# Optimization experiments

Hardware: AMD Instinct MI355X
Metric: run time of the kernel (lower is better)

Reference implementation:

```python
import jax, jax.numpy as jnp
import numpy as np

# Dimensions
B2, T, C = 400, 120, 128          # x: ((B*V), T, C)
V = 25                            # num_point (skeleton joints)
NH_A = 3                          # adjacency heads (A.shape[0])
HEADS, DH = 8, 64                 # attention heads, dim_head
INNER = HEADS * DH                # 512
QKV_C = INNER * 3                 # 1536 = GCN out_channels
EPS = 1e-5                        # torch BatchNorm2d default eps


def setup_inputs() -> dict:
    key = jax.random.key(0)
    ks = jax.random.split(key, 12)
    z = lambda *s: jnp.zeros(s, jnp.float32)
    o = lambda *s: jnp.ones(s, jnp.float32)
    return {
        "x": jax.random.normal(ks[0], (B2, T, C), jnp.float32),
        # GCN shared topology (num_head, V, V)
        "A": jax.random.normal(ks[1], (NH_A, V, V), jnp.float32) * 0.2,
        # per-head 1x1 conv weights/biases (stacked)
        "conv_w": jax.random.normal(ks[2], (NH_A, QKV_C, C), jnp.float32) * 0.02,
        "conv_b": jax.random.normal(ks[3], (NH_A, QKV_C), jnp.float32) * 0.01,
        # main BatchNorm2d (eval mode, running stats)
        "bn_gamma": jax.random.uniform(ks[4], (QKV_C,), jnp.float32, 0.5, 1.5),
        "bn_beta": z(QKV_C),
        "bn_mean": z(QKV_C),
        "bn_var": o(QKV_C),
        # down path: 1x1 conv + BatchNorm2d (in_c != out_c)
        "down_w": jax.random.normal(ks[5], (QKV_C, C), jnp.float32) * 0.02,
        "down_b": z(QKV_C),
        "dbn_gamma": jax.random.uniform(ks[6], (QKV_C,), jnp.float32, 0.5, 1.5),
        "dbn_beta": z(QKV_C),
        "dbn_mean": z(QKV_C),
        "dbn_var": o(QKV_C),
        # to_out Linear(inner_dim -> dim)
        "out_w": jax.random.normal(ks[7], (C, INNER), jnp.float32) * 0.02,
        "out_b": z(C),
    }


def _bn_eval(y, gamma, beta, mean, var):
    # y: (b, o, t, v); BN over channel axis 1, eval mode
    inv = gamma / jnp.sqrt(var + EPS)
    return y * inv[None, :, None, None] + (beta - mean * inv)[None, :, None, None]


def reference(x, A, conv_w, conv_b, bn_gamma, bn_beta, bn_mean, bn_var,
              down_w, down_b, dbn_gamma, dbn_beta, dbn_mean, dbn_var,
              out_w, out_b):
    B = B2 // V
    # '(b v) t c -> b c t v'
    x4 = x.reshape(B, V, T, C).transpose(0, 3, 2, 1)  # (b, c, t, v)

    # ---- GCN projection: sum_h Conv1x1_h(A_h @ x) ----
    z = jnp.einsum('hvu,bctu->bhctv', A, x4)                    # (b,h,c,t,v)
    y = jnp.einsum('hoc,bhctv->botv', conv_w, z)                # (b,O,t,v)
    y = y + conv_b.sum(0)[None, :, None, None]
    y = _bn_eval(y, bn_gamma, bn_beta, bn_mean, bn_var)

    d = jnp.einsum('oc,bctv->botv', down_w, x4) + down_b[None, :, None, None]
    d = _bn_eval(d, dbn_gamma, dbn_beta, dbn_mean, dbn_var)

    y = jax.nn.relu(y + d)                                      # (b,O,t,v)

    # ---- attention over time per (batch*joint) row ----
    qkv = y.transpose(0, 3, 2, 1).reshape(B2, T, QKV_C)         # '(b v) t c'
    q, k, v = jnp.split(qkv, 3, axis=-1)
    split_heads = lambda t: t.reshape(B2, T, HEADS, DH).transpose(0, 2, 1, 3)
    q, k, v = split_heads(q), split_heads(k), split_heads(v)

    dots = jnp.einsum('bhid,bhjd->bhij', q, k) * (DH ** -0.5)
    mask = jnp.tril(jnp.ones((T, T), bool))                     # causal mask
    dots = jnp.where(mask[None, None], dots, -jnp.inf)
    attn = jax.nn.softmax(dots, axis=-1)                        # (B2,H,T,T)

    o = jnp.einsum('bhij,bhjd->bhid', attn, v)
    o = o.transpose(0, 2, 1, 3).reshape(B2, T, INNER)
    out = o @ out_w.T + out_b                                   # (B2,T,C)
    return out, attn
```

## Files before the change

kernel.cpp:

```cpp
#include <hip/hip_runtime.h>


typedef __bf16 bf16;
typedef __bf16 bf16x8 __attribute__((ext_vector_type(8)));
typedef __bf16 bf16x4 __attribute__((ext_vector_type(4)));
typedef float  f32x4  __attribute__((ext_vector_type(4)));
typedef __attribute__((address_space(1))) const void* gptr1;
typedef __attribute__((address_space(3))) void*       lptr3;

#define GLL16(g, l) __builtin_amdgcn_global_load_lds((gptr1)(g), (lptr3)(l), 16, 0, 0)
#define MFMA16(a, b, c) __builtin_amdgcn_mfma_f32_16x16x32_bf16(a, b, c, 0, 0, 0)

__global__ __launch_bounds__(256) void build_weights(
    const float* __restrict__ conv_w, const float* __restrict__ conv_b,
    const float* __restrict__ g1, const float* __restrict__ be1,
    const float* __restrict__ mu1, const float* __restrict__ va1,
    const float* __restrict__ down_w, const float* __restrict__ down_b,
    const float* __restrict__ g2, const float* __restrict__ be2,
    const float* __restrict__ mu2, const float* __restrict__ va2,
    const float* __restrict__ out_w,
    bf16* __restrict__ wcat, bf16* __restrict__ wout, float* __restrict__ bias)
{
    int idx = blockIdx.x * 256 + threadIdx.x;
    if (idx < 1536 * 512) {
        int o = idx >> 9, k = idx & 511;
        float s, w;
        if (k < 384) {
            int h = k >> 7, c = k & 127;
            s = g1[o] * rsqrtf(va1[o] + 1e-5f);
            w = conv_w[(h * 1536 + o) * 128 + c];
        } else {
            s = g2[o] * rsqrtf(va2[o] + 1e-5f);
            w = down_w[o * 128 + (k - 384)];
        }
        wcat[idx] = (bf16)(w * s);
    }
    int i2 = idx - 1536 * 512;
    if (i2 >= 0 && i2 < 128 * 512) wout[i2] = (bf16)out_w[i2];
    int i3 = idx - (1536 * 512 + 128 * 512);
    if (i3 >= 0 && i3 < 1536) {
        int o = i3;
        float s1 = g1[o] * rsqrtf(va1[o] + 1e-5f);
        float s2 = g2[o] * rsqrtf(va2[o] + 1e-5f);
        float cb = conv_b[o] + conv_b[1536 + o] + conv_b[2 * 1536 + o];
        bias[o] = cb * s1 + be1[o] - mu1[o] * s1
                + down_b[o] * s2 + be2[o] - mu2[o] * s2;
    }
}

__global__ __launch_bounds__(256) void transform(
    const float* __restrict__ x, const float* __restrict__ A,
    bf16* __restrict__ zt)
{
    __shared__ float xs[25][128];
    const int tid = threadIdx.x;
    const int bt = blockIdx.x;
    const int b = bt / 120, t = bt - b * 120;
    for (int i = tid; i < 25 * 128; i += 256) {
        int u = i >> 7, c = i & 127;
        xs[u][c] = x[((size_t)(b * 25 + u) * 120 + t) * 128 + c];
    }
    __syncthreads();
    const int c = tid & 127, g = tid >> 7;
    float xr[25];
    #pragma unroll
    for (int u = 0; u < 25; u++) xr[u] = xs[u][c];
    for (int idx = g; idx < 75; idx += 2) {
        int h = idx / 25, v = idx - h * 25;
        const float* Ap = A + (h * 25 + v) * 25;
        float acc = 0.f;
        #pragma unroll
        for (int u = 0; u < 25; u++) acc += Ap[u] * xr[u];
        zt[((size_t)(b * 25 + v) * 120 + t) * 512 + h * 128 + c] = (bf16)acc;
    }
    for (int v = g; v < 25; v += 2)
        zt[((size_t)(b * 25 + v) * 120 + t) * 512 + 384 + c] = (bf16)xs[v][c];
}

__global__ __launch_bounds__(256) void gemm_qkv(
    const bf16* __restrict__ wcat, const bf16* __restrict__ zt,
    const float* __restrict__ bias,
    bf16* __restrict__ qg, bf16* __restrict__ kg, bf16* __restrict__ vtg)
{
    __shared__ __align__(16) char smem[32768];
    bf16* AsB = (bf16*)smem;
    bf16* BsB = (bf16*)(smem + 8192);
    const int tid = threadIdx.x, lane = tid & 63, wv = tid >> 6;
    const int wrow = wv >> 1, wcol = wv & 1;
    const int NB = 4500, q8 = NB >> 3, r8 = NB & 7;
    const int xcd = blockIdx.x & 7, sidx = blockIdx.x >> 3;
    const int vid = (xcd < r8 ? xcd * (q8 + 1) : r8 * (q8 + 1) + (xcd - r8) * q8) + sidx;
    const int mt = vid % 12, nt = vid / 12;
    const int colb = lane & 15, rg = lane >> 4;

    f32x4 zz = {0.f, 0.f, 0.f, 0.f};
    f32x4 acc[4][4];
    #pragma unroll
    for (int i = 0; i < 4; i++)
        #pragma unroll
        for (int j = 0; j < 4; j++) acc[i][j] = zz;

    const char* gA = (const char*)wcat + (size_t)mt * 128 * 1024;
    const char* gB = (const char*)zt + (size_t)nt * 128 * 1024;
    const int srow = lane >> 2, skb = (lane & 3) * 16;
    const int aoff0 = (wrow * 64 + colb) * 64 + rg * 16;
    const int boff0 = (wcol * 64 + colb) * 64 + rg * 16;

    for (int kt = 0; kt < 16; kt++) {
        __syncthreads();
        #pragma unroll
        for (int j = 0; j < 2; j++) {
            int ck = wv * 2 + j;
            int row = ck * 16 + srow;
            GLL16(gA + (size_t)row * 1024 + kt * 64 + skb, (char*)AsB + ck * 1024);
            GLL16(gB + (size_t)row * 1024 + kt * 64 + skb, (char*)BsB + ck * 1024);
        }
        asm volatile("s_waitcnt vmcnt(0)" ::: "memory");
        __syncthreads();
        bf16x8 af[4], bfr[4];
        #pragma unroll
        for (int m = 0; m < 4; m++)
            af[m] = *(const bf16x8*)((const char*)AsB + aoff0 + m * 1024);
        #pragma unroll
        for (int n = 0; n < 4; n++)
            bfr[n] = *(const bf16x8*)((const char*)BsB + boff0 + n * 1024);
        #pragma unroll
        for (int m = 0; m < 4; m++)
            #pragma unroll
            for (int n = 0; n < 4; n++)
                acc[m][n] = MFMA16(af[m], bfr[n], acc[m][n]);
    }

    const int mtb = mt * 128, ntb = nt * 128;
    const int which = mtb >> 9;

    if (which < 2) {
        __syncthreads();
        bf16* Lt = (bf16*)smem;
        const float qs = (which == 0) ? 0.125f : 1.0f;
        #pragma unroll
        for (int m = 0; m < 4; m++) {
            int o0 = wrow * 64 + m * 16 + rg * 4;
            float b0 = bias[mtb + o0 + 0], b1 = bias[mtb + o0 + 1];
            float b2 = bias[mtb + o0 + 2], b3 = bias[mtb + o0 + 3];
            #pragma unroll
            for (int nn = 0; nn < 4; nn++) {
                int n_ = wcol * 64 + nn * 16 + colb;
                bf16x4 pk;
                pk[0] = (bf16)(fmaxf(acc[m][nn][0] + b0, 0.f) * qs);
                pk[1] = (bf16)(fmaxf(acc[m][nn][1] + b1, 0.f) * qs);
                pk[2] = (bf16)(fmaxf(acc[m][nn][2] + b2, 0.f) * qs);
                pk[3] = (bf16)(fmaxf(acc[m][nn][3] + b3, 0.f) * qs);
                *(bf16x4*)((char*)Lt + n_ * 256 + ((o0 * 2) ^ ((n_ & 7) << 4))) = pk;
            }
        }
        __syncthreads();
        bf16* dst = (which == 0) ? qg : kg;
        #pragma unroll
        for (int i = 0; i < 8; i++) {
            int ch = i * 256 + tid;
            int n_ = ch >> 4, c16 = ch & 15;
            int ng = ntb + n_;
            int grp = ng / 120, t = ng - grp * 120;
            int o = mtb + c16 * 8;
            int hd = (o >> 6) & 7, dd0 = o & 63;
            bf16x8 vv = *(const bf16x8*)((const char*)Lt + n_ * 256 +
                                         ((c16 * 16) ^ ((n_ & 7) << 4)));
            *(bf16x8*)(dst + ((size_t)(grp * 8 + hd) * 120 + t) * 64 + dd0) = vv;
        }
    } else {
        #pragma unroll
        for (int m = 0; m < 4; m++) {
            #pragma unroll
            for (int reg = 0; reg < 4; reg++) {
                int o = mtb + wrow * 64 + m * 16 + rg * 4 + reg;
                float bo = bias[o];
                int hd = (o >> 6) & 7, dd = o & 63;
                #pragma unroll
                for (int nn = 0; nn < 4; nn++) {
                    int n = ntb + wcol * 64 + nn * 16 + colb;
                    int grp = n / 120, t = n - grp * 120;
                    float val = fmaxf(acc[m][nn][reg] + bo, 0.f);
                    vtg[((size_t)(grp * 8 + hd) * 64 + dd) * 128 + t] = (bf16)val;
                }
            }
        }
    }
}

__global__ __launch_bounds__(256) void attn_k(
    const bf16* __restrict__ qg, const bf16* __restrict__ kg,
    const bf16* __restrict__ vtg, float* __restrict__ attn_out,
    bf16* __restrict__ og)
{
    __shared__ __align__(16) bf16 Ks[128 * 64];
    __shared__ __align__(16) bf16 Vt[64 * 128];
    __shared__ __align__(16) bf16 Ps[128 * 128];
    const int tid = threadIdx.x, lane = tid & 63, wv = tid >> 6;
    const int bh = blockIdx.x;
    const int colb = lane & 15, rg = lane >> 4;

    const char* ksrc = (const char*)kg + (size_t)bh * 15360;
    const char* vsrc = (const char*)vtg + (size_t)bh * 16384;
    #pragma unroll
    for (int is = 0; is < 4; is++) {
        int cb = is * 256 + wv * 64;
        if (cb < 960) {
            int bb = (cb + lane) * 16;
            int row = bb >> 7;
            int gsrc = (bb & ~127) | ((bb & 127) ^ ((row & 7) << 4));
            GLL16(ksrc + gsrc, (char*)Ks + cb * 16);
        }
        {
            int bb = (cb + lane) * 16;
            int row = bb >> 8;
            int gsrc = (bb & ~255) | ((bb & 255) ^ ((row & 7) << 4));
            GLL16(vsrc + gsrc, (char*)Vt + cb * 16);
        }
    }
    const char* qsrc = (const char*)qg + (size_t)bh * 15360;
    bf16x8 qf[2][2];
    #pragma unroll
    for (int kk = 0; kk < 2; kk++)
        #pragma unroll
        for (int m = 0; m < 2; m++) {
            int row = wv * 32 + m * 16 + colb;
            qf[kk][m] = *(const bf16x8*)(qsrc + (size_t)row * 128 + rg * 16 + kk * 64);
        }
    asm volatile("s_waitcnt vmcnt(0)" ::: "memory");
    __syncthreads();
    {
        f32x4 z = {0.f, 0.f, 0.f, 0.f};
        if (tid < 64) {
            int r = 120 + (tid >> 3), off = (tid & 7) * 16;
            *(f32x4*)((char*)Ks + r * 128 + off) = z;
        } else if (tid < 128) {
            int d = tid - 64;
            *(f32x4*)((char*)Vt + d * 256 + (240 ^ ((d & 7) << 4))) = z;
        }
    }
    __syncthreads();

    f32x4 accs[2][8];
    #pragma unroll
    for (int m = 0; m < 2; m++)
        #pragma unroll
        for (int ct = 0; ct < 8; ct++) accs[m][ct] = (f32x4){0.f, 0.f, 0.f, 0.f};
    #pragma unroll
    for (int kk = 0; kk < 2; kk++) {
        #pragma unroll
        for (int ct = 0; ct < 8; ct++) {
            int rk = ct * 16 + colb;
            int byo = rk * 128 + ((rg * 16 + kk * 64) ^ ((rk & 7) << 4));
            bf16x8 bk = *(const bf16x8*)((const char*)Ks + byo);
            accs[0][ct] = MFMA16(qf[kk][0], bk, accs[0][ct]);
            accs[1][ct] = MFMA16(qf[kk][1], bk, accs[1][ct]);
        }
    }

    const int rqb = wv * 32;
    float* attn_base = attn_out + (size_t)bh * 120 * 120;
    #pragma unroll
    for (int m = 0; m < 2; m++) {
        #pragma unroll
        for (int reg = 0; reg < 4; reg++) {
            int t_q = rqb + m * 16 + rg * 4 + reg;
            float s[8], mx = -1e30f;
            #pragma unroll
            for (int ct = 0; ct < 8; ct++) {
                int col = ct * 16 + colb;
                bool valid = (col <= t_q) && (col < 120);
                s[ct] = valid ? accs[m][ct][reg] : -1e30f;
                mx = fmaxf(mx, s[ct]);
            }
            #pragma unroll
            for (int d = 1; d < 16; d <<= 1) mx = fmaxf(mx, __shfl_xor(mx, d, 64));
            float p[8], sum = 0.f;
            #pragma unroll
            for (int ct = 0; ct < 8; ct++) {
                p[ct] = (s[ct] > -1e29f) ? __expf(s[ct] - mx) : 0.f;
                sum += p[ct];
            }
            #pragma unroll
            for (int d = 1; d < 16; d <<= 1) sum += __shfl_xor(sum, d, 64);
            float inv = 1.f / sum;
            if (t_q < 120) {
                float* orow = attn_base + (size_t)t_q * 120;
                #pragma unroll
                for (int ct = 0; ct < 8; ct++) {
                    int col = ct * 16 + colb;
                    if (col < 120) orow[col] = p[ct] * inv;
                }
            }
            #pragma unroll
            for (int ct = 0; ct < 8; ct++) {
                int col = ct * 16 + colb;
                int byo = t_q * 256 + ((col * 2) ^ ((t_q & 7) << 4));
                *(bf16*)((char*)Ps + byo) = (bf16)(p[ct] * inv);
            }
        }
    }
    __syncthreads();

    f32x4 acco[2][4];
    #pragma unroll
    for (int m = 0; m < 2; m++)
        #pragma unroll
        for (int dt = 0; dt < 4; dt++) acco[m][dt] = (f32x4){0.f, 0.f, 0.f, 0.f};
    for (int kk = 0; kk <= wv; kk++) {
        bf16x8 ap[2];
        #pragma unroll
        for (int m = 0; m < 2; m++) {
            int row = rqb + m * 16 + colb;
            int byo = row * 256 + ((rg * 16 + kk * 64) ^ ((row & 7) << 4));
            ap[m] = *(const bf16x8*)((const char*)Ps + byo);
        }
        #pragma unroll
        for (int dt = 0; dt < 4; dt++) {
            int rd = dt * 16 + colb;
            int byo = rd * 256 + ((rg * 16 + kk * 64) ^ ((rd & 7) << 4));
            bf16x8 bv = *(const bf16x8*)((const char*)Vt + byo);
            acco[0][dt] = MFMA16(ap[0], bv, acco[0][dt]);
            acco[1][dt] = MFMA16(ap[1], bv, acco[1][dt]);
        }
    }
    const int b2 = bh >> 3, h = bh & 7;
    #pragma unroll
    for (int m = 0; m < 2; m++)
        #pragma unroll
        for (int dt = 0; dt < 4; dt++)
            #pragma unroll
            for (int reg = 0; reg < 4; reg++) {
                int t = rqb + m * 16 + rg * 4 + reg;
                if (t < 120) {
                    int dfull = h * 64 + dt * 16 + colb;
                    og[((size_t)b2 * 120 + t) * 512 + dfull] = (bf16)acco[m][dt][reg];
                }
            }
}

__global__ __launch_bounds__(256) void gemm_out_k(
    const bf16* __restrict__ og, const bf16* __restrict__ wout,
    const float* __restrict__ outb, float* __restrict__ out)
{
    __shared__ __align__(16) bf16 As[128 * 32];
    __shared__ __align__(16) bf16 Bs[128 * 32];
    const int tid = threadIdx.x, lane = tid & 63, wv = tid >> 6;
    const int wrow = wv >> 1, wcol = wv & 1;
    const int nt = blockIdx.x;
    const int colb = lane & 15, rg = lane >> 4;

    f32x4 zz = {0.f, 0.f, 0.f, 0.f};
    f32x4 acc[4][4];
    #pragma unroll
    for (int i = 0; i < 4; i++)
        #pragma unroll
        for (int j = 0; j < 4; j++) acc[i][j] = zz;

    const char* gA = (const char*)og + (size_t)nt * 128 * 1024;
    const char* gB = (const char*)wout;
    const int srow = lane >> 2, skb = (lane & 3) * 16;
    const int aoff0 = (wrow * 64 + colb) * 64 + rg * 16;
    const int boff0 = (wcol * 64 + colb) * 64 + rg * 16;

    for (int kt = 0; kt < 16; kt++) {
        __syncthreads();
        #pragma unroll
        for (int j = 0; j < 2; j++) {
            int ck = wv * 2 + j;
            int row = ck * 16 + srow;
            GLL16(gA + (size_t)row * 1024 + kt * 64 + skb, (char*)As + ck * 1024);
            GLL16(gB + (size_t)row * 1024 + kt * 64 + skb, (char*)Bs + ck * 1024);
        }
        asm volatile("s_waitcnt vmcnt(0)" ::: "memory");
        __syncthreads();
        bf16x8 af[4], bfr[4];
        #pragma unroll
        for (int m = 0; m < 4; m++)
            af[m] = *(const bf16x8*)((const char*)As + aoff0 + m * 1024);
        #pragma unroll
        for (int n = 0; n < 4; n++)
            bfr[n] = *(const bf16x8*)((const char*)Bs + boff0 + n * 1024);
        #pragma unroll
        for (int m = 0; m < 4; m++)
            #pragma unroll
            for (int n = 0; n < 4; n++)
                acc[m][n] = MFMA16(af[m], bfr[n], acc[m][n]);
    }

    const int rbase = nt * 128 + wrow * 64;
    #pragma unroll
    for (int m = 0; m < 4; m++)
        #pragma unroll
        for (int reg = 0; reg < 4; reg++) {
            int r = rbase + m * 16 + rg * 4 + reg;
            #pragma unroll
            for (int nn = 0; nn < 4; nn++) {
                int c = wcol * 64 + nn * 16 + colb;
                out[(size_t)r * 128 + c] = acc[m][nn][reg] + outb[c];
            }
        }
}

extern "C" void kernel_launch(void* const* d_in, const int* in_sizes, int n_in,
                              void* d_out, int out_size, void* d_ws, size_t ws_size,
                              hipStream_t stream)
{
    (void)in_sizes; (void)n_in; (void)out_size; (void)ws_size;
    const float* x      = (const float*)d_in[0];
    const float* A      = (const float*)d_in[1];
    const float* conv_w = (const float*)d_in[2];
    const float* conv_b = (const float*)d_in[3];
    const float* bn_g   = (const float*)d_in[4];
    const float* bn_b   = (const float*)d_in[5];
    const float* bn_m   = (const float*)d_in[6];
    const float* bn_v   = (const float*)d_in[7];
    const float* dw     = (const float*)d_in[8];
    const float* db     = (const float*)d_in[9];
    const float* dg     = (const float*)d_in[10];
    const float* dbb    = (const float*)d_in[11];
    const float* dm     = (const float*)d_in[12];
    const float* dvv    = (const float*)d_in[13];
    const float* out_w  = (const float*)d_in[14];
    const float* out_b  = (const float*)d_in[15];

    char* ws = (char*)d_ws;
    const size_t OFF_WCAT = 0;
    const size_t OFF_WOUT = 1572864;
    const size_t OFF_BIAS = 1703936;
    const size_t OFF_ZT   = 1710080;
    const size_t OFF_Q    = 50862080;
    const size_t OFF_K    = 100014080;
    const size_t OFF_VT   = 149166080;
    const size_t OFF_O    = OFF_ZT;

    bf16*  wcat = (bf16*)(ws + OFF_WCAT);
    bf16*  wout = (bf16*)(ws + OFF_WOUT);
    float* bias = (float*)(ws + OFF_BIAS);
    bf16*  zt   = (bf16*)(ws + OFF_ZT);
    bf16*  qg   = (bf16*)(ws + OFF_Q);
    bf16*  kg   = (bf16*)(ws + OFF_K);
    bf16*  vtg  = (bf16*)(ws + OFF_VT);
    bf16*  og   = (bf16*)(ws + OFF_O);
    float* outp = (float*)d_out;
    float* attn = outp + 6144000;

    build_weights<<<3334, 256, 0, stream>>>(conv_w, conv_b, bn_g, bn_b, bn_m, bn_v,
                                            dw, db, dg, dbb, dm, dvv, out_w,
                                            wcat, wout, bias);
    transform<<<1920, 256, 0, stream>>>(x, A, zt);
    gemm_qkv<<<4500, 256, 0, stream>>>(wcat, zt, bias, qg, kg, vtg);
    attn_k<<<3200, 256, 0, stream>>>(qg, kg, vtg, attn, og);
    gemm_out_k<<<375, 256, 0, stream>>>(og, wout, out_b, outp);
}
```

Measured before the change: 311.8 us.

## Triple-buffer GEMM LDS staging with async prefetch and single barrier per k-step

Both bf16 GEMM kernels (QKV projection and output projection) now use a three-stage LDS ring. Global-to-LDS loads for k-tile kt+2 are issued while tile kt is consumed, which replaces the load, wait-all, double-syncthreads pattern with a partial vmcnt wait and one barrier per iteration. MFMA sections are wrapped in s_setprio to favour matrix issue. Shared memory grows to 48KB per block, which can reduce occupancy. The attention kernel also aliases Ps onto the K buffer, adding a barrier so its LDS footprint matches the other kernels.

```diff
diff --git a/kernel.cpp b/kernel.cpp
--- a/kernel.cpp
+++ b/kernel.cpp
@@ -82,9 +82,7 @@
     const float* __restrict__ bias,
     bf16* __restrict__ qg, bf16* __restrict__ kg, bf16* __restrict__ vtg)
 {
-    __shared__ __align__(16) char smem[32768];
-    bf16* AsB = (bf16*)smem;
-    bf16* BsB = (bf16*)(smem + 8192);
+    __shared__ __align__(16) char smem[49152];
     const int tid = threadIdx.x, lane = tid & 63, wv = tid >> 6;
     const int wrow = wv >> 1, wcol = wv & 1;
     const int NB = 4500, q8 = NB >> 3, r8 = NB & 7;
@@ -106,36 +104,47 @@
     const int aoff0 = (wrow * 64 + colb) * 64 + rg * 16;
     const int boff0 = (wcol * 64 + colb) * 64 + rg * 16;
 
+    #define STAGE_QKV(kt, b) do {                                              \
+        char* As_ = smem + (b) * 16384; char* Bs_ = As_ + 8192;                \
+        _Pragma("unroll")                                                      \
+        for (int j = 0; j < 2; j++) {                                          \
+            int ck = wv * 2 + j;  int row = ck * 16 + srow;                    \
+            GLL16(gA + (size_t)row * 1024 + (kt) * 64 + skb, As_ + ck * 1024); \
+            GLL16(gB + (size_t)row * 1024 + (kt) * 64 + skb, Bs_ + ck * 1024); \
+        } } while (0)
+
+    STAGE_QKV(0, 0);
+    STAGE_QKV(1, 1);
+    asm volatile("s_waitcnt vmcnt(4)" ::: "memory");
+    __builtin_amdgcn_s_barrier();
     for (int kt = 0; kt < 16; kt++) {
-        __syncthreads();
-        #pragma unroll
-        for (int j = 0; j < 2; j++) {
-            int ck = wv * 2 + j;
-            int row = ck * 16 + srow;
-            GLL16(gA + (size_t)row * 1024 + kt * 64 + skb, (char*)AsB + ck * 1024);
-            GLL16(gB + (size_t)row * 1024 + kt * 64 + skb, (char*)BsB + ck * 1024);
-        }
-        asm volatile("s_waitcnt vmcnt(0)" ::: "memory");
-        __syncthreads();
+        const char* As = smem + (kt % 3) * 16384;
+        const char* Bs = As + 8192;
         bf16x8 af[4], bfr[4];
         #pragma unroll
         for (int m = 0; m < 4; m++)
-            af[m] = *(const bf16x8*)((const char*)AsB + aoff0 + m * 1024);
+            af[m] = *(const bf16x8*)(As + aoff0 + m * 1024);
         #pragma unroll
         for (int n = 0; n < 4; n++)
-            bfr[n] = *(const bf16x8*)((const char*)BsB + boff0 + n * 1024);
+            bfr[n] = *(const bf16x8*)(Bs + boff0 + n * 1024);
+        int kn = kt + 2;
+        STAGE_QKV(kn < 16 ? kn : 15, kn % 3);
+        __builtin_amdgcn_s_setprio(1);
         #pragma unroll
         for (int m = 0; m < 4; m++)
             #pragma unroll
             for (int n = 0; n < 4; n++)
                 acc[m][n] = MFMA16(af[m], bfr[n], acc[m][n]);
-    }
+        __builtin_amdgcn_s_setprio(0);
+        asm volatile("s_waitcnt vmcnt(4)" ::: "memory");
+        __builtin_amdgcn_s_barrier();
+    }
+    __builtin_amdgcn_sched_barrier(0);
 
     const int mtb = mt * 128, ntb = nt * 128;
     const int which = mtb >> 9;
 
     if (which < 2) {
-        __syncthreads();
         bf16* Lt = (bf16*)smem;
         const float qs = (which == 0) ? 0.125f : 1.0f;
         #pragma unroll
@@ -186,6 +195,7 @@
             }
         }
     }
+    #undef STAGE_QKV
 }
 
 __global__ __launch_bounds__(256) void attn_k(
@@ -193,9 +203,10 @@
     const bf16* __restrict__ vtg, float* __restrict__ attn_out,
     bf16* __restrict__ og)
 {
-    __shared__ __align__(16) bf16 Ks[128 * 64];
-    __shared__ __align__(16) bf16 Vt[64 * 128];
-    __shared__ __align__(16) bf16 Ps[128 * 128];
+    __shared__ __align__(16) char sm[49152];
+    char* Vt = sm;
+    char* Ks = sm + 16384;
+    char* Ps = sm + 16384;
     const int tid = threadIdx.x, lane = tid & 63, wv = tid >> 6;
     const int bh = blockIdx.x;
     const int colb = lane & 15, rg = lane >> 4;
@@ -209,13 +220,13 @@
             int bb = (cb + lane) * 16;
             int row = bb >> 7;
             int gsrc = (bb & ~127) | ((bb & 127) ^ ((row & 7) << 4));
-            GLL16(ksrc + gsrc, (char*)Ks + cb * 16);
+            GLL16(ksrc + gsrc, Ks + cb * 16);
         }
         {
             int bb = (cb + lane) * 16;
             int row = bb >> 8;
             int gsrc = (bb & ~255) | ((bb & 255) ^ ((row & 7) << 4));
-            GLL16(vsrc + gsrc, (char*)Vt + cb * 16);
+            GLL16(vsrc + gsrc, Vt + cb * 16);
         }
     }
     const char* qsrc = (const char*)qg + (size_t)bh * 15360;
@@ -233,10 +244,10 @@
         f32x4 z = {0.f, 0.f, 0.f, 0.f};
         if (tid < 64) {
             int r = 120 + (tid >> 3), off = (tid & 7) * 16;
-            *(f32x4*)((char*)Ks + r * 128 + off) = z;
+            *(f32x4*)(Ks + r * 128 + off) = z;
         } else if (tid < 128) {
             int d = tid - 64;
-            *(f32x4*)((char*)Vt + d * 256 + (240 ^ ((d & 7) << 4))) = z;
+            *(f32x4*)(Vt + d * 256 + (240 ^ ((d & 7) << 4))) = z;
         }
     }
     __syncthreads();
@@ -252,11 +263,12 @@
         for (int ct = 0; ct < 8; ct++) {
             int rk = ct * 16 + colb;
             int byo = rk * 128 + ((rg * 16 + kk * 64) ^ ((rk & 7) << 4));
-            bf16x8 bk = *(const bf16x8*)((const char*)Ks + byo);
+            bf16x8 bk = *(const bf16x8*)(Ks + byo);
             accs[0][ct] = MFMA16(qf[kk][0], bk, accs[0][ct]);
             accs[1][ct] = MFMA16(qf[kk][1], bk, accs[1][ct]);
         }
     }
+    __syncthreads();
 
     const int rqb = wv * 32;
     float* attn_base = attn_out + (size_t)bh * 120 * 120;
@@ -296,7 +308,7 @@
             for (int ct = 0; ct < 8; ct++) {
                 int col = ct * 16 + colb;
                 int byo = t_q * 256 + ((col * 2) ^ ((t_q & 7) << 4));
-                *(bf16*)((char*)Ps + byo) = (bf16)(p[ct] * inv);
+                *(bf16*)(Ps + byo) = (bf16)(p[ct] * inv);
             }
         }
     }
@@ -313,13 +325,13 @@
         for (int m = 0; m < 2; m++) {
             int row = rqb + m * 16 + colb;
             int byo = row * 256 + ((rg * 16 + kk * 64) ^ ((row & 7) << 4));
-            ap[m] = *(const bf16x8*)((const char*)Ps + byo);
+            ap[m] = *(const bf16x8*)(Ps + byo);
         }
         #pragma unroll
         for (int dt = 0; dt < 4; dt++) {
             int rd = dt * 16 + colb;
             int byo = rd * 256 + ((rg * 16 + kk * 64) ^ ((rd & 7) << 4));
-            bf16x8 bv = *(const bf16x8*)((const char*)Vt + byo);
+            bf16x8 bv = *(const bf16x8*)(Vt + byo);
             acco[0][dt] = MFMA16(ap[0], bv, acco[0][dt]);
             acco[1][dt] = MFMA16(ap[1], bv, acco[1][dt]);
         }
@@ -343,8 +355,7 @@
     const bf16* __restrict__ og, const bf16* __restrict__ wout,
     const float* __restrict__ outb, float* __restrict__ out)
 {
-    __shared__ __align__(16) bf16 As[128 * 32];
-    __shared__ __align__(16) bf16 Bs[128 * 32];
+    __shared__ __align__(16) char smem[49152];
     const int tid = threadIdx.x, lane = tid & 63, wv = tid >> 6;
     const int wrow = wv >> 1, wcol = wv & 1;
     const int nt = blockIdx.x;
@@ -363,30 +374,42 @@
     const int aoff0 = (wrow * 64 + colb) * 64 + rg * 16;
     const int boff0 = (wcol * 64 + colb) * 64 + rg * 16;
 
+    #define STAGE_OUT(kt, b) do {                                              \
+        char* As_ = smem + (b) * 16384; char* Bs_ = As_ + 8192;                \
+        _Pragma("unroll")                                                      \
+        for (int j = 0; j < 2; j++) {                                          \
+            int ck = wv * 2 + j;  int row = ck * 16 + srow;                    \
+            GLL16(gA + (size_t)row * 1024 + (kt) * 64 + skb, As_ + ck * 1024); \
+            GLL16(gB + (size_t)row * 1024 + (kt) * 64 + skb, Bs_ + ck * 1024); \
+        } } while (0)
+
+    STAGE_OUT(0, 0);
+    STAGE_OUT(1, 1);
+    asm volatile("s_waitcnt vmcnt(4)" ::: "memory");
+    __builtin_amdgcn_s_barrier();
     for (int kt = 0; kt < 16; kt++) {
-        __syncthreads();
-        #pragma unroll
-        for (int j = 0; j < 2; j++) {
-            int ck = wv * 2 + j;
-            int row = ck * 16 + srow;
-            GLL16(gA + (size_t)row * 1024 + kt * 64 + skb, (char*)As + ck * 1024);
-            GLL16(gB + (size_t)row * 1024 + kt * 64 + skb, (char*)Bs + ck * 1024);
-        }
-        asm volatile("s_waitcnt vmcnt(0)" ::: "memory");
-        __syncthreads();
+        const char* As = smem + (kt % 3) * 16384;
+        const char* Bs = As + 8192;
         bf16x8 af[4], bfr[4];
         #pragma unroll
         for (int m = 0; m < 4; m++)
-            af[m] = *(const bf16x8*)((const char*)As + aoff0 + m * 1024);
+            af[m] = *(const bf16x8*)(As + aoff0 + m * 1024);
         #pragma unroll
         for (int n = 0; n < 4; n++)
-            bfr[n] = *(const bf16x8*)((const char*)Bs + boff0 + n * 1024);
+            bfr[n] = *(const bf16x8*)(Bs + boff0 + n * 1024);
+        int kn = kt + 2;
+        STAGE_OUT(kn < 16 ? kn : 15, kn % 3);
+        __builtin_amdgcn_s_setprio(1);
         #pragma unroll
         for (int m = 0; m < 4; m++)
             #pragma unroll
             for (int n = 0; n < 4; n++)
                 acc[m][n] = MFMA16(af[m], bfr[n], acc[m][n]);
-    }
+        __builtin_amdgcn_s_setprio(0);
+        asm volatile("s_waitcnt vmcnt(4)" ::: "memory");
+        __builtin_amdgcn_s_barrier();
+    }
+    __builtin_amdgcn_sched_barrier(0);
 
     const int rbase = nt * 128 + wrow * 64;
     #pragma unroll
@@ -400,6 +423,7 @@
                 out[(size_t)r * 128 + c] = acc[m][nn][reg] + outb[c];
             }
         }
+    #undef STAGE_OUT
 }
 
 extern "C" void kernel_launch(void* const* d_in, const int* in_sizes, int n_in,
```

Result: faster. 284.2 us (-8.8%).
